# Optimization experiments

Hardware: AMD Instinct MI355X
Metric: run time of the kernel (lower is better)

The kernel has to match this reference:

```python
import jax, jax.numpy as jnp
import numpy as np

B, S, D, H, FFN = 8, 1024, 1024, 16, 4096
DH = D // H  # per-head dim = 64
NEG = -1e9
EPS = 1e-5


def layer_norm(x):
    # F.layer_norm over last dim, no affine params (matches add_and_norm_dropout)
    mu = jnp.mean(x, axis=-1, keepdims=True)
    var = jnp.var(x, axis=-1, keepdims=True)
    return (x - mu) / jnp.sqrt(var + EPS)


def setup_inputs() -> dict:
    key = jax.random.key(0)
    ks = jax.random.split(key, 10)
    scale = 1.0 / np.sqrt(D)
    x = jax.random.normal(ks[0], (B, S, D), dtype=jnp.float32)
    real_lengths = jax.random.randint(ks[1], (B,), 1, S + 1)
    # per-head projection weights stacked: [H, D, DH] (nn.Linear(D, DH, bias=False) per head)
    Wq = jax.random.uniform(ks[2], (H, D, DH), jnp.float32, -scale, scale)
    Wk = jax.random.uniform(ks[3], (H, D, DH), jnp.float32, -scale, scale)
    Wv = jax.random.uniform(ks[4], (H, D, DH), jnp.float32, -scale, scale)
    Wo = jax.random.uniform(ks[5], (D, H * DH), jnp.float32, -scale, scale)  # Linear(H*DH, D, bias=False)
    W1 = jax.random.uniform(ks[6], (FFN, D), jnp.float32, -scale, scale)
    b1 = jax.random.uniform(ks[7], (FFN,), jnp.float32, -scale, scale)
    s2 = 1.0 / np.sqrt(FFN)
    W2 = jax.random.uniform(ks[8], (D, FFN), jnp.float32, -s2, s2)
    b2 = jax.random.uniform(ks[9], (D,), jnp.float32, -s2, s2)
    return {"x": x, "real_lengths": real_lengths, "Wq": Wq, "Wk": Wk, "Wv": Wv,
            "Wo": Wo, "W1": W1, "b1": b1, "W2": W2, "b2": b2}


def reference(x, real_lengths, Wq, Wk, Wv, Wo, W1, b1, W2, b2):
    b, s, d = x.shape
    # padding mask: True where key position >= real_length (masked out)
    key_pad = jnp.arange(s)[None, :] >= real_lengths[:, None]  # [B, S]

    # batched per-head projections (equivalent to the Python per-head loop)
    q = jnp.einsum('bsd,hde->bhse', x, Wq)
    k = jnp.einsum('bsd,hde->bhse', x, Wk)
    v = jnp.einsum('bsd,hde->bhse', x, Wv)

    scores = jnp.einsum('bhse,bhte->bhst', q, k) / jnp.sqrt(jnp.float32(DH))
    scores = jnp.where(key_pad[:, None, None, :], NEG, scores)
    attn = jax.nn.softmax(scores, axis=-1)
    heads = jnp.einsum('bhst,bhte->bhse', attn, v)       # [B,H,S,DH]
    concat = heads.transpose(0, 2, 1, 3).reshape(b, s, d)  # head concat
    attn_out = concat @ Wo.T

    x1 = layer_norm(x + attn_out)  # add & norm (eval: no dropout)

    ffn = jax.nn.relu(x1 @ W1.T + b1) @ W2.T + b2
    return layer_norm(x1 + ffn)
```

## Files before the change

### kernel.cpp

```cpp
#include <hip/hip_runtime.h>
#include <hip/hip_bf16.h>
#include <math.h>

#define B_ 8
#define S_ 1024
#define D_ 1024
#define H_ 16
#define DH_ 64
#define FFN_ 4096
#define NEG_ (-1e9f)
#define EPS_ 1e-5f

typedef float f32x4 __attribute__((ext_vector_type(4)));
typedef short bf16x8 __attribute__((ext_vector_type(8)));

__device__ __forceinline__ ushort f2b(float f) {
  __hip_bfloat16 h = __float2bfloat16(f);
  return *reinterpret_cast<ushort*>(&h);
}
__device__ __forceinline__ float b2f(ushort u) {
  return __uint_as_float((unsigned)u << 16);
}

__device__ __forceinline__ void gload16(const void* g, void* l) {
  auto* lp = (__attribute__((address_space(3))) unsigned*)(uintptr_t)(l);
  __builtin_amdgcn_global_load_lds(
      (const __attribute__((address_space(1))) unsigned*)g, lp, 16, 0, 0);
}

__device__ __forceinline__ void* swz_ptr(void* base, int row, int col) {
  int byte = (row << 7) + (col << 1);
  byte ^= (row & 7) << 4;
  return (char*)base + byte;
}

#define BARR asm volatile("s_barrier" ::: "memory")
#define LGKM0                                         \
  do {                                                \
    asm volatile("s_waitcnt lgkmcnt(0)" ::: "memory"); \
    __builtin_amdgcn_sched_barrier(0);                \
  } while (0)

__global__ __launch_bounds__(256) void prep_k(
    const float* __restrict__ x, const float* __restrict__ Wq,
    const float* __restrict__ Wk, const float* __restrict__ Wv,
    const float* __restrict__ Wo, const float* __restrict__ W1,
    const float* __restrict__ W2, ushort* __restrict__ xbf,
    ushort* __restrict__ qkvw, ushort* __restrict__ wob,
    ushort* __restrict__ w1b, ushort* __restrict__ w2b) {
  const int blk = blockIdx.x, t = threadIdx.x;
  if (blk < 8192) {
    int i = blk * 256 + t;
    float4 v = ((const float4*)x)[i];
    ushort4 o;
    o.x = f2b(v.x); o.y = f2b(v.y); o.z = f2b(v.z); o.w = f2b(v.w);
    ((ushort4*)xbf)[i] = o;
  } else if (blk < 8192 + 12288) {
    int idx = (blk - 8192) * 256 + t;
    int e = idx & 63, k = (idx >> 6) & 1023;
    int h = (idx >> 16) & 15, which = idx >> 20;
    const float* W = (which == 0) ? Wq : (which == 1 ? Wk : Wv);
    float v = W[((size_t)h * D_ + k) * DH_ + e];
    qkvw[((size_t)which * 1024 + h * 64 + e) * 1024 + k] = f2b(v);
  } else if (blk < 8192 + 12288 + 1024) {
    int i = (blk - 8192 - 12288) * 256 + t;
    float4 v = ((const float4*)Wo)[i];
    ushort4 o;
    o.x = f2b(v.x); o.y = f2b(v.y); o.z = f2b(v.z); o.w = f2b(v.w);
    ((ushort4*)wob)[i] = o;
  } else if (blk < 8192 + 12288 + 1024 + 4096) {
    int i = (blk - 8192 - 12288 - 1024) * 256 + t;
    float4 v = ((const float4*)W1)[i];
    ushort4 o;
    o.x = f2b(v.x); o.y = f2b(v.y); o.z = f2b(v.z); o.w = f2b(v.w);
    ((ushort4*)w1b)[i] = o;
  } else {
    int i = (blk - 8192 - 12288 - 1024 - 4096) * 256 + t;
    float4 v = ((const float4*)W2)[i];
    ushort4 o;
    o.x = f2b(v.x); o.y = f2b(v.y); o.z = f2b(v.z); o.w = f2b(v.w);
    ((ushort4*)w2b)[i] = o;
  }
}

template <int BIAS, int RELU, int VSPLIT>
__global__ __launch_bounds__(512, 2) void gemm8p(
    const ushort* __restrict__ A, const ushort* __restrict__ Bt,
    const float* __restrict__ bias, ushort* __restrict__ C,
    ushort* __restrict__ vT, int M, int N, int K) {
  __shared__ ushort lds[2][2][2][256 * 32];
  const int nbn = N >> 8;
  const int nwg = gridDim.x;
  const int cpx = nwg >> 3;
  const int bid = blockIdx.x;
  const int swz = (bid & 7) * cpx + (bid >> 3);
  const int bm = swz / nbn, bn = swz % nbn;

  const int t = threadIdx.x;
  const int lane = t & 63, lr = lane & 15, lg = lane >> 4;
  const int wid = t >> 6, wr = wid >> 2, wc = wid & 3;
  const size_t Kb = (size_t)K * 2;
  const char* Ab = (const char*)A + ((size_t)(bm << 8)) * Kb;
  const char* Bb = (const char*)Bt + ((size_t)(bn << 8)) * Kb;
  const int NT = K >> 6;
  const int niter = NT >> 1;

  const int g0row = t >> 2;
  const int gsi = (t & 3) ^ (g0row & 3);
  auto STG = [&](int mat, int kh, int kt) {
    char* base = (char*)&lds[kt & 1][mat][kh][0];
    const char* gsrc = mat ? Bb : Ab;
#pragma unroll
    for (int j = 0; j < 2; j++) {
      int row = g0row + j * 128;
      const char* src = gsrc + (size_t)row * Kb +
                        (size_t)(kt * 64 + kh * 32) * 2 + gsi * 16;
      gload16(src, base + t * 16 + j * 8192);
    }
  };

  const int rg = (lg ^ (lr & 3)) << 3;
#define LDA(DST, BUF, KH, QM)                                            \
  _Pragma("unroll") for (int mm = 0; mm < 4; mm++) {                     \
    int row = wr * 128 + (QM)*64 + mm * 16 + lr;                         \
    DST[mm] = *(const bf16x8*)&lds[BUF][0][KH][row * 32 + rg];           \
  }
#define LDB(DST, BUF, KH)                                                \
  _Pragma("unroll") for (int nn = 0; nn < 4; nn++) {                     \
    int row = wc * 64 + nn * 16 + lr;                                    \
    DST[nn] = *(const bf16x8*)&lds[BUF][1][KH][row * 32 + rg];           \
  }
#define MFQ(QM, AS, BS)                                                  \
  do {                                                                   \
    __builtin_amdgcn_s_setprio(1);                                       \
    _Pragma("unroll") for (int mm = 0; mm < 4; mm++)                     \
        _Pragma("unroll") for (int nn = 0; nn < 4; nn++)                 \
            acc[(QM)*4 + mm][nn] = __builtin_amdgcn_mfma_f32_16x16x32_bf16( \
                AS[mm], BS[nn], acc[(QM)*4 + mm][nn], 0, 0, 0);          \
    __builtin_amdgcn_s_setprio(0);                                       \
  } while (0)

  f32x4 acc[8][4] = {};
  bf16x8 aS0[4], aS1[4], bS0[4], bS1[4];

  STG(0, 0, 0); STG(1, 0, 0); STG(0, 1, 0); STG(1, 1, 0);
  STG(0, 0, 1); STG(1, 0, 1);
  asm volatile("s_waitcnt vmcnt(4)" ::: "memory");
  BARR;

  for (int i = 0; i < niter; i++) {
    const int c1 = 2 * i + 1, c2 = 2 * i + 2, c3 = 2 * i + 3;
    LDA(aS0, 0, 0, 0); LDB(bS0, 0, 0); STG(0, 1, c1);
    BARR; LGKM0; MFQ(0, aS0, bS0); BARR;
    LDA(aS1, 0, 0, 1); STG(1, 1, c1);
    BARR; LGKM0; MFQ(1, aS1, bS0); BARR;
    LDA(aS0, 0, 1, 0); LDB(bS1, 0, 1);
    if (c2 < NT) STG(0, 0, c2);
    BARR; LGKM0; MFQ(0, aS0, bS1); BARR;
    LDA(aS1, 0, 1, 1);
    if (c2 < NT) STG(1, 0, c2);
    BARR; LGKM0; MFQ(1, aS1, bS1);
    if (i + 1 < niter)
      asm volatile("s_waitcnt vmcnt(4)" ::: "memory");
    else
      asm volatile("s_waitcnt vmcnt(0)" ::: "memory");
    BARR;
    LDA(aS0, 1, 0, 0); LDB(bS0, 1, 0);
    if (c2 < NT) STG(0, 1, c2);
    BARR; LGKM0; MFQ(0, aS0, bS0); BARR;
    LDA(aS1, 1, 0, 1);
    if (c2 < NT) STG(1, 1, c2);
    BARR; LGKM0; MFQ(1, aS1, bS0); BARR;
    LDA(aS0, 1, 1, 0); LDB(bS1, 1, 1);
    if (c3 < NT) STG(0, 0, c3);
    BARR; LGKM0; MFQ(0, aS0, bS1); BARR;
    LDA(aS1, 1, 1, 1);
    if (c3 < NT) STG(1, 0, c3);
    BARR; LGKM0; MFQ(1, aS1, bS1);
    asm volatile("s_waitcnt vmcnt(4)" ::: "memory");
    BARR;
  }
#undef LDA
#undef LDB
#undef MFQ

  const int r0 = (bm << 8) + wr * 128 + lg * 4;
  const int c0 = (bn << 8) + wc * 64 + lr;
#pragma unroll
  for (int m = 0; m < 8; m++) {
#pragma unroll
    for (int n = 0; n < 4; n++) {
      int col = c0 + n * 16;
      float bv = BIAS ? bias[col] : 0.0f;
      if (VSPLIT && col >= 2048) {
        int row = r0 + m * 16;
        int hh = (col - 2048) >> 6, e = col & 63;
        ushort4 uv;
        uv.x = f2b(acc[m][n][0]); uv.y = f2b(acc[m][n][1]);
        uv.z = f2b(acc[m][n][2]); uv.w = f2b(acc[m][n][3]);
        *(ushort4*)&vT[((((size_t)(row >> 10) * 16 + hh) * 64 + e) << 10) +
                       (row & 1023)] = uv;
      } else {
#pragma unroll
        for (int q = 0; q < 4; q++) {
          int row = r0 + m * 16 + q;
          float v = acc[m][n][q] + bv;
          if (RELU) v = fmaxf(v, 0.0f);
          if (VSPLIT)
            C[(size_t)row * 2048 + col] = f2b(v);
          else
            C[(size_t)row * N + col] = f2b(v);
        }
      }
    }
  }
}

template <int BIAS, int RELU>
__global__ __launch_bounds__(256) void gemm_bf16(
    const ushort* __restrict__ A, const ushort* __restrict__ Bt,
    const float* __restrict__ bias, ushort* __restrict__ C,
    int M, int N, int K) {
  __shared__ ushort Al[2][128 * 64];
  __shared__ ushort Bl[2][128 * 64];
  const int nb = N >> 7;
  const int bm = blockIdx.x / nb, bn = blockIdx.x % nb;
  const int t = threadIdx.x;
  const int lane = t & 63;
  const int wid = t >> 6, wr = wid >> 1, wc = wid & 1;
  const int row0 = bm << 7, col0 = bn << 7;
  const size_t Kb = (size_t)K * 2;
  const int NT = K >> 6;

  const char* Abase = (const char*)A + (size_t)row0 * Kb;
  const char* Bbase = (const char*)Bt + (size_t)col0 * Kb;

  f32x4 acc[4][4] = {};
  const int o0 = t * 16;
  const int lrow = lane & 15, lkb = (lane >> 4) * 8;

  auto STAGE = [&](int buf, int kt) {
#pragma unroll
    for (int i = 0; i < 4; i++) {
      int ob = o0 + i * 4096;
      int row = ob >> 7, inrow = ob & 127;
      const char* ga = Abase + (size_t)row * Kb + kt * 128 + inrow;
      const char* gb = Bbase + (size_t)row * Kb + kt * 128 + inrow;
      gload16(ga, (char*)&Al[buf][0] + ob);
      gload16(gb, (char*)&Bl[buf][0] + ob);
    }
  };
  auto COMPUTE = [&](int buf) {
#pragma unroll
    for (int kk = 0; kk < 64; kk += 32) {
      bf16x8 af[4], bfr[4];
      const int lk = lkb + kk;
#pragma unroll
      for (int m = 0; m < 4; m++)
        af[m] = *(const bf16x8*)&Al[buf][(wr * 64 + m * 16 + lrow) * 64 + lk];
#pragma unroll
      for (int n = 0; n < 4; n++)
        bfr[n] = *(const bf16x8*)&Bl[buf][(wc * 64 + n * 16 + lrow) * 64 + lk];
#pragma unroll
      for (int m = 0; m < 4; m++)
#pragma unroll
        for (int n = 0; n < 4; n++)
          acc[m][n] = __builtin_amdgcn_mfma_f32_16x16x32_bf16(
              af[m], bfr[n], acc[m][n], 0, 0, 0);
    }
  };

  STAGE(0, 0);
  __syncthreads();
  int cur = 0;
  for (int kt = 1; kt < NT; kt++) {
    STAGE(cur ^ 1, kt);
    COMPUTE(cur);
    __syncthreads();
    cur ^= 1;
  }
  COMPUTE(cur);

  const int rbase = row0 + wr * 64 + (lane >> 4) * 4;
  const int cbase = col0 + wc * 64 + (lane & 15);
#pragma unroll
  for (int m = 0; m < 4; m++) {
#pragma unroll
    for (int n = 0; n < 4; n++) {
      int col = cbase + n * 16;
      float bv = BIAS ? bias[col] : 0.0f;
#pragma unroll
      for (int q = 0; q < 4; q++) {
        int row = rbase + m * 16 + q;
        float v = acc[m][n][q] + bv;
        if (RELU) v = fmaxf(v, 0.0f);
        C[(size_t)row * N + col] = f2b(v);
      }
    }
  }
}

__global__ __launch_bounds__(256) void attention_mfma_k(
    const ushort* __restrict__ qk, const ushort* __restrict__ vT,
    const int* __restrict__ lens, ushort* __restrict__ concat) {
  __shared__ ushort Qs[64 * 64];
  __shared__ ushort Ks[64 * 64];
  __shared__ ushort Vt[64 * 64];
  __shared__ ushort Pl[4][16 * 64];
  const int blk = blockIdx.x;
  const int b = blk & 7, h = (blk >> 3) & 15, q0 = (blk >> 7) << 6;
  const int t = threadIdx.x;
  const int lane = t & 63, w = t >> 6;
  const int lr = lane & 15, lg = lane >> 4;
  const int lg4 = lg * 4;
  const int len_b = lens[b];
  ushort* Plw = &Pl[w][0];
  const ushort* vbase = vT + ((size_t)(b * 16 + h) << 16);

#pragma unroll
  for (int i = 0; i < 4; i++) {
    int idx = t + i * 256;
    int r = idx >> 4, eq = idx & 15;
    const ushort* src =
        qk + ((size_t)(b * S_ + q0 + r)) * 2048 + h * 64 + eq * 4;
    *(ushort4*)swz_ptr(Qs, r, eq * 4) = *(const ushort4*)src;
  }
  __syncthreads();
  bf16x8 qf[2];
#pragma unroll
  for (int ds = 0; ds < 2; ds++)
    qf[ds] = *(const bf16x8*)swz_ptr(Qs, w * 16 + lr, lg * 8 + ds * 32);

  float mrun = -INFINITY, lrun = 0.f;
  f32x4 o[4] = {};

  ushort4 kreg[4], vreg[4];
  auto LOADT = [&](int j0) {
#pragma unroll
    for (int i = 0; i < 4; i++) {
      int idx = t + i * 256;
      int r = idx >> 4, eq = idx & 15;
      kreg[i] = *(const ushort4*)(qk + ((size_t)(b * S_ + j0 + r)) * 2048 +
                                  1024 + h * 64 + eq * 4);
      vreg[i] = *(const ushort4*)(vbase + (size_t)r * 1024 + j0 + eq * 4);
    }
  };

  const int ntiles = (len_b + 63) >> 6;
  LOADT(0);
  for (int jt = 0; jt < ntiles; jt++) {
    const int j0 = jt << 6;
    __syncthreads();
#pragma unroll
    for (int i = 0; i < 4; i++) {
      int idx = t + i * 256;
      int r = idx >> 4, eq = idx & 15;
      *(ushort4*)swz_ptr(Ks, r, eq * 4) = kreg[i];
      *(ushort4*)swz_ptr(Vt, r, eq * 4) = vreg[i];
    }
    if (jt + 1 < ntiles) LOADT(j0 + 64);
    __syncthreads();

    f32x4 sacc[4];
    __builtin_amdgcn_s_setprio(1);
#pragma unroll
    for (int mb = 0; mb < 4; mb++) {
      sacc[mb] = (f32x4){0.f, 0.f, 0.f, 0.f};
#pragma unroll
      for (int ds = 0; ds < 2; ds++) {
        bf16x8 kf = *(const bf16x8*)swz_ptr(Ks, mb * 16 + lr, lg * 8 + ds * 32);
        sacc[mb] = __builtin_amdgcn_mfma_f32_16x16x32_bf16(kf, qf[ds], sacc[mb],
                                                           0, 0, 0);
      }
    }
    __builtin_amdgcn_s_setprio(0);

    float p[4][4];
    float pmax = -INFINITY;
#pragma unroll
    for (int mb = 0; mb < 4; mb++)
#pragma unroll
      for (int qi = 0; qi < 4; qi++) {
        float v = sacc[mb][qi] * 0.125f;
        if (j0 + mb * 16 + lg4 + qi >= len_b) v = NEG_;
        p[mb][qi] = v;
        pmax = fmaxf(pmax, v);
      }
    pmax = fmaxf(pmax, __shfl_xor(pmax, 16));
    pmax = fmaxf(pmax, __shfl_xor(pmax, 32));
    if (!__all(pmax - mrun <= 8.0f)) {
      float mnew = fmaxf(mrun, pmax);
      float sc = __expf(mrun - mnew);
      mrun = mnew;
      lrun *= sc;
#pragma unroll
      for (int qi = 0; qi < 4; qi++) {
        float scq = __shfl(sc, (lg << 4) + lg4 + qi);
#pragma unroll
        for (int dt = 0; dt < 4; dt++) o[dt][qi] *= scq;
      }
    }
    float rs = 0.f;
#pragma unroll
    for (int mb = 0; mb < 4; mb++)
#pragma unroll
      for (int qi = 0; qi < 4; qi++) {
        float e = __expf(p[mb][qi] - mrun);
        p[mb][qi] = e;
        rs += e;
      }
    rs += __shfl_xor(rs, 16);
    rs += __shfl_xor(rs, 32);
    lrun += rs;

#pragma unroll
    for (int mb = 0; mb < 4; mb++) {
      ushort2 w0, w1;
      w0.x = f2b(p[mb][0]); w0.y = f2b(p[mb][1]);
      w1.x = f2b(p[mb][2]); w1.y = f2b(p[mb][3]);
      *(ushort2*)swz_ptr(Plw, lr, mb * 16 + lg4) = w0;
      *(ushort2*)swz_ptr(Plw, lr, mb * 16 + lg4 + 2) = w1;
    }

    bf16x8 pf[2];
#pragma unroll
    for (int ks = 0; ks < 2; ks++)
      pf[ks] = *(const bf16x8*)swz_ptr(Plw, lr, lg * 8 + ks * 32);
    __builtin_amdgcn_s_setprio(1);
#pragma unroll
    for (int dt = 0; dt < 4; dt++) {
#pragma unroll
      for (int ks = 0; ks < 2; ks++) {
        bf16x8 vf = *(const bf16x8*)swz_ptr(Vt, dt * 16 + lr, lg * 8 + ks * 32);
        o[dt] = __builtin_amdgcn_mfma_f32_16x16x32_bf16(pf[ks], vf, o[dt],
                                                        0, 0, 0);
      }
    }
    __builtin_amdgcn_s_setprio(0);
  }

#pragma unroll
  for (int qi = 0; qi < 4; qi++) {
    float lq = __shfl(lrun, (lg << 4) + lg4 + qi);
    float inv = 1.0f / lq;
    size_t row = (size_t)(b * S_ + q0 + w * 16 + lg4 + qi);
#pragma unroll
    for (int dt = 0; dt < 4; dt++)
      concat[row * 1024 + h * 64 + dt * 16 + lr] = f2b(o[dt][qi] * inv);
  }
}

template <int WBF>
__global__ __launch_bounds__(256) void add_ln_k(const float* __restrict__ a,
                                                const ushort* __restrict__ r,
                                                float* __restrict__ y,
                                                ushort* __restrict__ yb) {
  const int row = blockIdx.x, t = threadIdx.x;
  const float4 av = ((const float4*)(a + (size_t)row * 1024))[t];
  const ushort4 rv = ((const ushort4*)(r + (size_t)row * 1024))[t];
  float v[4] = {av.x + b2f(rv.x), av.y + b2f(rv.y), av.z + b2f(rv.z),
                av.w + b2f(rv.w)};
  float s = v[0] + v[1] + v[2] + v[3];
  float q = v[0] * v[0] + v[1] * v[1] + v[2] * v[2] + v[3] * v[3];
#pragma unroll
  for (int off = 1; off < 64; off <<= 1) {
    s += __shfl_xor(s, off);
    q += __shfl_xor(q, off);
  }
  __shared__ float ss[4], sq[4];
  int wave = t >> 6, lane = t & 63;
  if (lane == 0) { ss[wave] = s; sq[wave] = q; }
  __syncthreads();
  s = ss[0] + ss[1] + ss[2] + ss[3];
  q = sq[0] + sq[1] + sq[2] + sq[3];
  float mean = s * (1.f / 1024.f);
  float var = q * (1.f / 1024.f) - mean * mean;
  float inv = 1.0f / sqrtf(var + EPS_);
  float4 yo;
  yo.x = (v[0] - mean) * inv; yo.y = (v[1] - mean) * inv;
  yo.z = (v[2] - mean) * inv; yo.w = (v[3] - mean) * inv;
  ((float4*)(y + (size_t)row * 1024))[t] = yo;
  if (WBF) {
    ushort4 ob;
    ob.x = f2b(yo.x); ob.y = f2b(yo.y); ob.z = f2b(yo.z); ob.w = f2b(yo.w);
    ((ushort4*)(yb + (size_t)row * 1024))[t] = ob;
  }
}

extern "C" void kernel_launch(void* const* d_in, const int* in_sizes, int n_in,
                              void* d_out, int out_size, void* d_ws, size_t ws_size,
                              hipStream_t stream) {
  const float* x  = (const float*)d_in[0];
  const int* len  = (const int*)d_in[1];
  const float* Wq = (const float*)d_in[2];
  const float* Wk = (const float*)d_in[3];
  const float* Wv = (const float*)d_in[4];
  const float* Wo = (const float*)d_in[5];
  const float* W1 = (const float*)d_in[6];
  const float* b1 = (const float*)d_in[7];
  const float* W2 = (const float*)d_in[8];
  const float* b2 = (const float*)d_in[9];
  float* out = (float*)d_out;

  if (ws_size < (size_t)184 * 1024 * 1024) return;
  char* w = (char*)d_ws;
  ushort* xbf    = (ushort*)(w);
  ushort* qkvw   = (ushort*)(w + ((size_t)16 << 20));
  ushort* wob    = (ushort*)(w + ((size_t)22 << 20));
  ushort* w1b    = (ushort*)(w + ((size_t)24 << 20));
  ushort* w2b    = (ushort*)(w + ((size_t)32 << 20));
  ushort* qk2    = (ushort*)(w + ((size_t)40 << 20));
  ushort* vT     = (ushort*)(w + ((size_t)72 << 20));
  ushort* concat = (ushort*)(w + ((size_t)88 << 20));
  ushort* attno  = (ushort*)(w + ((size_t)104 << 20));
  float*  x1     = (float*) (w + ((size_t)136 << 20));
  ushort* x1b    = (ushort*)(w + ((size_t)168 << 20));
  ushort* hidden = (ushort*)(w + ((size_t)40 << 20));
  ushort* ffn2o  = (ushort*)(w + ((size_t)104 << 20));

  prep_k<<<29696, 256, 0, stream>>>(x, Wq, Wk, Wv, Wo, W1, W2,
                                    xbf, qkvw, wob, w1b, w2b);

  gemm8p<0, 0, 1><<<32 * 12, 512, 0, stream>>>(xbf, qkvw, nullptr, qk2,
                                               vT, 8192, 3072, 1024);
  attention_mfma_k<<<2048, 256, 0, stream>>>(qk2, vT, len, concat);
  gemm_bf16<0, 0><<<64 * 8, 256, 0, stream>>>(concat, wob, nullptr, attno,
                                              8192, 1024, 1024);
  add_ln_k<1><<<8192, 256, 0, stream>>>(x, attno, x1, x1b);
  gemm8p<1, 1, 0><<<32 * 16, 512, 0, stream>>>(x1b, w1b, b1, hidden,
                                               nullptr, 8192, 4096, 1024);
  gemm_bf16<1, 0><<<64 * 8, 256, 0, stream>>>(hidden, w2b, b2, ffn2o,
                                              8192, 1024, 4096);
  add_ln_k<0><<<8192, 256, 0, stream>>>(x1, ffn2o, out, nullptr);
}
```

Baseline: 386.2 us.

## Widen attention key tile to 128 and remap GEMM blocks across XCDs

The attention kernel now processes 128 keys per iteration instead of 64, with larger K/V/P shared buffers and a new 256-byte-row swizzle. This halves the loop iterations, barriers and softmax rescale checks per query block. The GEMM kernel remaps block IDs so consecutive tiles land on the same XCD chiplet, aiming for better L2 reuse. The costs are more registers and LDS in attention, which may lower occupancy, and extra wasted work on padded keys when a sequence length is just past a 128 boundary.

```diff
diff --git a/kernel.cpp b/kernel.cpp
--- a/kernel.cpp
+++ b/kernel.cpp
@@ -30,6 +30,11 @@
 
 __device__ __forceinline__ void* swz_ptr(void* base, int row, int col) {
   int byte = (row << 7) + (col << 1);
+  byte ^= (row & 7) << 4;
+  return (char*)base + byte;
+}
+__device__ __forceinline__ void* swz256(void* base, int row, int col) {
+  int byte = (row << 8) + (col << 1);
   byte ^= (row & 7) << 4;
   return (char*)base + byte;
 }
@@ -224,7 +229,11 @@
   __shared__ ushort Al[2][128 * 64];
   __shared__ ushort Bl[2][128 * 64];
   const int nb = N >> 7;
-  const int bm = blockIdx.x / nb, bn = blockIdx.x % nb;
+  const int nwg = gridDim.x;
+  const int cpx = nwg >> 3;
+  const int bid = blockIdx.x;
+  const int swb = (bid & 7) * cpx + (bid >> 3);
+  const int bm = swb / nb, bn = swb % nb;
   const int t = threadIdx.x;
   const int lane = t & 63;
   const int wid = t >> 6, wr = wid >> 1, wc = wid & 1;
@@ -304,9 +313,9 @@
     const ushort* __restrict__ qk, const ushort* __restrict__ vT,
     const int* __restrict__ lens, ushort* __restrict__ concat) {
   __shared__ ushort Qs[64 * 64];
-  __shared__ ushort Ks[64 * 64];
-  __shared__ ushort Vt[64 * 64];
-  __shared__ ushort Pl[4][16 * 64];
+  __shared__ ushort Ks[128 * 64];
+  __shared__ ushort Vt[64 * 128];
+  __shared__ ushort Pl[4][16 * 128];
   const int blk = blockIdx.x;
   const int b = blk & 7, h = (blk >> 3) & 15, q0 = (blk >> 7) << 6;
   const int t = threadIdx.x;
@@ -334,37 +343,39 @@
   float mrun = -INFINITY, lrun = 0.f;
   f32x4 o[4] = {};
 
-  ushort4 kreg[4], vreg[4];
+  ushort4 kreg[8], vreg[8];
   auto LOADT = [&](int j0) {
 #pragma unroll
-    for (int i = 0; i < 4; i++) {
+    for (int i = 0; i < 8; i++) {
       int idx = t + i * 256;
-      int r = idx >> 4, eq = idx & 15;
-      kreg[i] = *(const ushort4*)(qk + ((size_t)(b * S_ + j0 + r)) * 2048 +
-                                  1024 + h * 64 + eq * 4);
-      vreg[i] = *(const ushort4*)(vbase + (size_t)r * 1024 + j0 + eq * 4);
+      int kr = idx >> 4, keq = idx & 15;
+      kreg[i] = *(const ushort4*)(qk + ((size_t)(b * S_ + j0 + kr)) * 2048 +
+                                  1024 + h * 64 + keq * 4);
+      int vr = idx >> 5, vc = idx & 31;
+      vreg[i] = *(const ushort4*)(vbase + (size_t)vr * 1024 + j0 + vc * 4);
     }
   };
 
-  const int ntiles = (len_b + 63) >> 6;
+  const int ntiles = (len_b + 127) >> 7;
   LOADT(0);
   for (int jt = 0; jt < ntiles; jt++) {
-    const int j0 = jt << 6;
+    const int j0 = jt << 7;
     __syncthreads();
 #pragma unroll
-    for (int i = 0; i < 4; i++) {
+    for (int i = 0; i < 8; i++) {
       int idx = t + i * 256;
-      int r = idx >> 4, eq = idx & 15;
-      *(ushort4*)swz_ptr(Ks, r, eq * 4) = kreg[i];
-      *(ushort4*)swz_ptr(Vt, r, eq * 4) = vreg[i];
-    }
-    if (jt + 1 < ntiles) LOADT(j0 + 64);
+      int kr = idx >> 4, keq = idx & 15;
+      *(ushort4*)swz_ptr(Ks, kr, keq * 4) = kreg[i];
+      int vr = idx >> 5, vc = idx & 31;
+      *(ushort4*)swz256(Vt, vr, vc * 4) = vreg[i];
+    }
+    if (jt + 1 < ntiles) LOADT(j0 + 128);
     __syncthreads();
 
-    f32x4 sacc[4];
+    f32x4 sacc[8];
     __builtin_amdgcn_s_setprio(1);
 #pragma unroll
-    for (int mb = 0; mb < 4; mb++) {
+    for (int mb = 0; mb < 8; mb++) {
       sacc[mb] = (f32x4){0.f, 0.f, 0.f, 0.f};
 #pragma unroll
       for (int ds = 0; ds < 2; ds++) {
@@ -375,10 +386,10 @@
     }
     __builtin_amdgcn_s_setprio(0);
 
-    float p[4][4];
+    float p[8][4];
     float pmax = -INFINITY;
 #pragma unroll
-    for (int mb = 0; mb < 4; mb++)
+    for (int mb = 0; mb < 8; mb++)
 #pragma unroll
       for (int qi = 0; qi < 4; qi++) {
         float v = sacc[mb][qi] * 0.125f;
@@ -402,7 +413,7 @@
     }
     float rs = 0.f;
 #pragma unroll
-    for (int mb = 0; mb < 4; mb++)
+    for (int mb = 0; mb < 8; mb++)
 #pragma unroll
       for (int qi = 0; qi < 4; qi++) {
         float e = __expf(p[mb][qi] - mrun);
@@ -414,24 +425,25 @@
     lrun += rs;
 
 #pragma unroll
-    for (int mb = 0; mb < 4; mb++) {
+    for (int mb = 0; mb < 8; mb++) {
       ushort2 w0, w1;
       w0.x = f2b(p[mb][0]); w0.y = f2b(p[mb][1]);
       w1.x = f2b(p[mb][2]); w1.y = f2b(p[mb][3]);
-      *(ushort2*)swz_ptr(Plw, lr, mb * 16 + lg4) = w0;
-      *(ushort2*)swz_ptr(Plw, lr, mb * 16 + lg4 + 2) = w1;
-    }
-
-    bf16x8 pf[2];
-#pragma unroll
-    for (int ks = 0; ks < 2; ks++)
-      pf[ks] = *(const bf16x8*)swz_ptr(Plw, lr, lg * 8 + ks * 32);
+      *(ushort2*)swz256(Plw, lr, mb * 16 + lg4) = w0;
+      *(ushort2*)swz256(Plw, lr, mb * 16 + lg4 + 2) = w1;
+    }
+
+    bf16x8 pf[4];
+#pragma unroll
+    for (int ks = 0; ks < 4; ks++)
+      pf[ks] = *(const bf16x8*)swz256(Plw, lr, lg * 8 + ks * 32);
     __builtin_amdgcn_s_setprio(1);
 #pragma unroll
     for (int dt = 0; dt < 4; dt++) {
 #pragma unroll
-      for (int ks = 0; ks < 2; ks++) {
-        bf16x8 vf = *(const bf16x8*)swz_ptr(Vt, dt * 16 + lr, lg * 8 + ks * 32);
+      for (int ks = 0; ks < 4; ks++) {
+        bf16x8 vf =
+            *(const bf16x8*)swz256(Vt, dt * 16 + lr, ks * 32 + lg * 8);
         o[dt] = __builtin_amdgcn_mfma_f32_16x16x32_bf16(pf[ks], vf, o[dt],
                                                         0, 0, 0);
       }
```

New measurement: 390.5 us. About the same (+1.1%).
